# Performance work log

Measured on AMD Instinct MI355X. Metric: run time of the kernel, lower is better.

## Reference

```python
import jax, jax.numpy as jnp
import numpy as np

EPS = 1e-8  # torch.nn.CosineSimilarity default eps


def setup_inputs() -> dict:
    key = jax.random.key(0)
    k1, k2, k3 = jax.random.split(key, 3)
    B, T, D, L = 16, 256, 512, 32
    v1 = jax.random.normal(k1, (B, T, D), dtype=jnp.float32)
    v1_mask = jnp.ones((B, T), dtype=jnp.float32)
    v2 = jax.random.normal(k2, (B, D), dtype=jnp.float32)
    w = jax.random.normal(k3, (L, D), dtype=jnp.float32)
    return {"v1": v1, "v1_mask": v1_mask, "v2": v2, "w": w}


def reference(v1, v1_mask, v2, w):
    # v1: [B,T,D], v1_mask: [B,T], v2: [B,D], w: [L,D]
    # Original math: cos over D of (w * v1) and (w * v2), per perspective l.
    # Fused: (w_l*a)\cdot(w_l*b) = sum_d w[l,d]^2 a[d] b[d]; likewise for norms.
    v1m = v1 * v1_mask[:, :, None]              # [B,T,D]
    w2 = w * w                                   # [L,D]
    num = jnp.einsum('btd,ld,bd->btl', v1m, w2, v2)          # [B,T,L]
    n1 = jnp.sqrt(jnp.einsum('btd,ld->btl', v1m * v1m, w2))  # [B,T,L]
    n2 = jnp.sqrt(jnp.einsum('bd,ld->bl', v2 * v2, w2))      # [B,L]
    denom = jnp.maximum(n1 * n2[:, None, :], EPS)
    return num / denom                           # [B,T,L]
```

## Files before the change

### kernel.cpp

```cpp
#include <hip/hip_runtime.h>
#include <cstddef>

#define BB      16
#define TDIM    256
#define DDIM    512
#define LDIM    32
#define TROWS   16
#define NTHREADS 1024
#define EPSV    1e-8f

__global__ __launch_bounds__(NTHREADS, 1) void fullmatch_kernel(
    const float* __restrict__ v1,
    const float* __restrict__ v1_mask,
    const float* __restrict__ v2,
    const float* __restrict__ w,
    float* __restrict__ out)
{
    const int tid  = threadIdx.x;
    const int b    = blockIdx.x >> 4;
    const int tgrp = blockIdx.x & 15;
    const int t0b  = tgrp * TROWS;

    const int dq = tid & 31;
    const int l  = tid >> 5;

    __shared__ float v1s[TROWS][DDIM];
    __shared__ float otile[TROWS][LDIM];

    float4 w2r[4], hr[4];
    float n2p = 0.f;
    {
        const float* __restrict__ wrow = w  + (size_t)l * DDIM;
        const float* __restrict__ v2b  = v2 + (size_t)b * DDIM;
        #pragma unroll
        for (int j = 0; j < 4; ++j) {
            const int d = dq * 4 + j * 128;
            const float4 wv = *(const float4*)(wrow + d);
            const float4 vv = *(const float4*)(v2b + d);
            float4 w2;
            w2.x = wv.x * wv.x; w2.y = wv.y * wv.y;
            w2.z = wv.z * wv.z; w2.w = wv.w * wv.w;
            w2r[j] = w2;
            float4 h;
            h.x = w2.x * vv.x; h.y = w2.y * vv.y;
            h.z = w2.z * vv.z; h.w = w2.w * vv.w;
            hr[j] = h;
            n2p = fmaf(h.x, vv.x, n2p);
            n2p = fmaf(h.y, vv.y, n2p);
            n2p = fmaf(h.z, vv.z, n2p);
            n2p = fmaf(h.w, vv.w, n2p);
        }
    }

    #pragma unroll
    for (int k = 0; k < 2; ++k) {
        const int f = tid + k * NTHREADS;
        const int r = f >> 7;
        const int q = f & 127;
        const float4 val = *(const float4*)(v1 + (size_t)(b * TDIM + t0b + r) * DDIM + q * 4);
        const float  mk  = v1_mask[b * TDIM + t0b + r];
        float4 o;
        o.x = val.x * mk; o.y = val.y * mk; o.z = val.z * mk; o.w = val.w * mk;
        *(float4*)(&v1s[r][q * 4]) = o;
    }
    __syncthreads();

    float accN[TROWS], accD[TROWS];
    #pragma unroll
    for (int t = 0; t < TROWS; ++t) { accN[t] = 0.f; accD[t] = 0.f; }

    #pragma unroll
    for (int j = 0; j < 4; ++j) {
        const float4 w2 = w2r[j];
        const float4 h  = hr[j];
        const float* __restrict__ base = &v1s[0][dq * 4 + j * 128];
        #pragma unroll
        for (int t = 0; t < TROWS; ++t) {
            const float4 a = *(const float4*)(base + t * DDIM);
            accN[t] = fmaf(a.x, h.x, accN[t]);
            accN[t] = fmaf(a.y, h.y, accN[t]);
            accN[t] = fmaf(a.z, h.z, accN[t]);
            accN[t] = fmaf(a.w, h.w, accN[t]);
            accD[t] = fmaf(a.x * a.x, w2.x, accD[t]);
            accD[t] = fmaf(a.y * a.y, w2.y, accD[t]);
            accD[t] = fmaf(a.z * a.z, w2.z, accD[t]);
            accD[t] = fmaf(a.w * a.w, w2.w, accD[t]);
        }
    }

    #pragma unroll
    for (int m = 16; m >= 1; m >>= 1) {
        n2p += __shfl_xor(n2p, m, 64);
        #pragma unroll
        for (int t = 0; t < TROWS; ++t) {
            accN[t] += __shfl_xor(accN[t], m, 64);
            accD[t] += __shfl_xor(accD[t], m, 64);
        }
    }

    if (dq == 0) {
        const float n2v = sqrtf(n2p);
        #pragma unroll
        for (int t = 0; t < TROWS; ++t) {
            const float den = fmaxf(sqrtf(accD[t]) * n2v, EPSV);
            otile[t][l] = accN[t] / den;
        }
    }
    __syncthreads();

    if (tid < (TROWS * LDIM) / 4) {
        const size_t base = (size_t)(b * TDIM + t0b) * LDIM;
        *(float4*)(out + base + tid * 4) = *(const float4*)(&otile[0][0] + tid * 4);
    }
}

extern "C" void kernel_launch(void* const* d_in, const int* in_sizes, int n_in,
                              void* d_out, int out_size, void* d_ws, size_t ws_size,
                              hipStream_t stream) {
    const float* v1      = (const float*)d_in[0];
    const float* v1_mask = (const float*)d_in[1];
    const float* v2      = (const float*)d_in[2];
    const float* w       = (const float*)d_in[3];
    float* out           = (float*)d_out;

    const dim3 grid(BB * (TDIM / TROWS));
    const dim3 block(NTHREADS);
    fullmatch_kernel<<<grid, block, 0, stream>>>(v1, v1_mask, v2, w, out);
}
```

Baseline: 21.73 us.

## Rewrite as thread-per-row kernel with async LDS double-buffering and readlane weight broadcast

Replaces the 1024-thread block with a 256-thread block where each lane owns one time row and each wave handles two perspectives. v1 is streamed in four D-chunks into double-buffered LDS using global_load_lds with an XOR swizzle, and the w^2 and h terms are broadcast with readlane. Because each lane accumulates its own row, the per-row cross-lane shuffle reduction goes away. The mask is applied algebraically in the epilogue, and block IDs are remapped so each XCD gets a group of tiles. The cost is that every block reloads the full v1 tile once for each of its four perspective groups, adding redundant global traffic, and the readlane-heavy inner loop puts more pressure on scalar registers.

```diff
diff --git a/kernel.cpp b/kernel.cpp
--- a/kernel.cpp
+++ b/kernel.cpp
@@ -1,15 +1,17 @@
 #include <hip/hip_runtime.h>
 #include <cstddef>
 
-#define BB      16
-#define TDIM    256
-#define DDIM    512
-#define LDIM    32
-#define TROWS   16
-#define NTHREADS 1024
-#define EPSV    1e-8f
+#define EPSV 1e-8f
 
-__global__ __launch_bounds__(NTHREADS, 1) void fullmatch_kernel(
+__device__ __forceinline__ float rdlane(float x, int s) {
+    return __int_as_float(__builtin_amdgcn_readlane(__float_as_int(x), s));
+}
+
+#define GLD16(gp, lp) \
+    __builtin_amdgcn_global_load_lds((const __attribute__((address_space(1))) void*)(gp), \
+                                     (__attribute__((address_space(3))) void*)(lp), 16, 0, 0)
+
+__global__ __launch_bounds__(256, 1) void fullmatch_kernel(
     const float* __restrict__ v1,
     const float* __restrict__ v1_mask,
     const float* __restrict__ v2,
@@ -17,101 +19,129 @@
     float* __restrict__ out)
 {
     const int tid  = threadIdx.x;
-    const int b    = blockIdx.x >> 4;
-    const int tgrp = blockIdx.x & 15;
-    const int t0b  = tgrp * TROWS;
+    const int lane = tid & 63;
+    const int wv   = tid >> 6;
 
-    const int dq = tid & 31;
-    const int l  = tid >> 5;
+    const int bid   = blockIdx.x;
+    const int xcd   = bid & 7;
+    const int slot  = bid >> 3;
+    const int tileg = xcd * 8 + (slot >> 2);
+    const int lg    = slot & 3;
+    const int b  = tileg >> 2;
+    const int tc = tileg & 3;
+    const int t0 = tc * 64;
+    const int p  = lg * 4 + wv;
+    const int t  = t0 + lane;
 
-    __shared__ float v1s[TROWS][DDIM];
-    __shared__ float otile[TROWS][LDIM];
+    __shared__ float v1s[2][64][128];
 
-    float4 w2r[4], hr[4];
-    float n2p = 0.f;
+    const size_t v1base = (size_t)(b * 256 + t0) * 512;
+
+    #pragma unroll
+    for (int j = 0; j < 8; ++j) {
+        const int r0 = (wv * 8 + j) * 2;
+        const int r  = r0 + (lane >> 5);
+        const int c4 = (lane & 31) ^ (r & 31);
+        GLD16(v1 + v1base + (size_t)r * 512 + c4 * 4, &v1s[0][r0][0]);
+    }
+
+    float4 w2A[2], w2B[2], hA[2], hB[2];
+    float n2pA = 0.f, n2pB = 0.f;
     {
-        const float* __restrict__ wrow = w  + (size_t)l * DDIM;
-        const float* __restrict__ v2b  = v2 + (size_t)b * DDIM;
+        const float* __restrict__ v2b = v2 + (size_t)b * 512;
+        const float* __restrict__ wAp = w + (size_t)p * 512;
+        const float* __restrict__ wBp = w + (size_t)(p + 16) * 512;
         #pragma unroll
-        for (int j = 0; j < 4; ++j) {
-            const int d = dq * 4 + j * 128;
-            const float4 wv = *(const float4*)(wrow + d);
-            const float4 vv = *(const float4*)(v2b + d);
-            float4 w2;
-            w2.x = wv.x * wv.x; w2.y = wv.y * wv.y;
-            w2.z = wv.z * wv.z; w2.w = wv.w * wv.w;
-            w2r[j] = w2;
-            float4 h;
-            h.x = w2.x * vv.x; h.y = w2.y * vv.y;
-            h.z = w2.z * vv.z; h.w = w2.w * vv.w;
-            hr[j] = h;
-            n2p = fmaf(h.x, vv.x, n2p);
-            n2p = fmaf(h.y, vv.y, n2p);
-            n2p = fmaf(h.z, vv.z, n2p);
-            n2p = fmaf(h.w, vv.w, n2p);
+        for (int q = 0; q < 2; ++q) {
+            const int k4 = q * 64 + lane;
+            const float4 wa = *(const float4*)(wAp + k4 * 4);
+            const float4 wb = *(const float4*)(wBp + k4 * 4);
+            const float4 vv = *(const float4*)(v2b + k4 * 4);
+            float4 sa, sb, ha, hb;
+            sa.x = wa.x*wa.x; sa.y = wa.y*wa.y; sa.z = wa.z*wa.z; sa.w = wa.w*wa.w;
+            sb.x = wb.x*wb.x; sb.y = wb.y*wb.y; sb.z = wb.z*wb.z; sb.w = wb.w*wb.w;
+            ha.x = sa.x*vv.x; ha.y = sa.y*vv.y; ha.z = sa.z*vv.z; ha.w = sa.w*vv.w;
+            hb.x = sb.x*vv.x; hb.y = sb.y*vv.y; hb.z = sb.z*vv.z; hb.w = sb.w*vv.w;
+            w2A[q] = sa; w2B[q] = sb; hA[q] = ha; hB[q] = hb;
+            n2pA += ha.x*vv.x + ha.y*vv.y + ha.z*vv.z + ha.w*vv.w;
+            n2pB += hb.x*vv.x + hb.y*vv.y + hb.z*vv.z + hb.w*vv.w;
+        }
+    }
+    #pragma unroll
+    for (int m = 32; m >= 1; m >>= 1) {
+        n2pA += __shfl_xor(n2pA, m, 64);
+        n2pB += __shfl_xor(n2pB, m, 64);
+    }
+    const float n2vA = sqrtf(n2pA);
+    const float n2vB = sqrtf(n2pB);
+    const float mk   = v1_mask[b * 256 + t];
+
+    float accNA = 0.f, accNB = 0.f, accDA = 0.f, accDB = 0.f;
+
+    #pragma unroll
+    for (int c = 0; c < 4; ++c) {
+        __syncthreads();
+        if (c < 3) {
+            #pragma unroll
+            for (int j = 0; j < 8; ++j) {
+                const int r0 = (wv * 8 + j) * 2;
+                const int r  = r0 + (lane >> 5);
+                const int c4 = (lane & 31) ^ (r & 31);
+                GLD16(v1 + v1base + (size_t)r * 512 + (c + 1) * 128 + c4 * 4,
+                      &v1s[(c + 1) & 1][r0][0]);
+            }
+        }
+        const float* __restrict__ row = &v1s[c & 1][lane][0];
+        const int lm = lane & 31;
+        #pragma unroll 8
+        for (int s = 0; s < 32; ++s) {
+            const float4 a = *(const float4*)(row + ((s ^ lm) << 2));
+            const int li = ((c & 1) << 5) + s;
+            const float wax = rdlane(w2A[c >> 1].x, li);
+            const float way = rdlane(w2A[c >> 1].y, li);
+            const float waz = rdlane(w2A[c >> 1].z, li);
+            const float waw = rdlane(w2A[c >> 1].w, li);
+            const float wbx = rdlane(w2B[c >> 1].x, li);
+            const float wby = rdlane(w2B[c >> 1].y, li);
+            const float wbz = rdlane(w2B[c >> 1].z, li);
+            const float wbw = rdlane(w2B[c >> 1].w, li);
+            const float hax = rdlane(hA[c >> 1].x, li);
+            const float hay = rdlane(hA[c >> 1].y, li);
+            const float haz = rdlane(hA[c >> 1].z, li);
+            const float haw = rdlane(hA[c >> 1].w, li);
+            const float hbx = rdlane(hB[c >> 1].x, li);
+            const float hby = rdlane(hB[c >> 1].y, li);
+            const float hbz = rdlane(hB[c >> 1].z, li);
+            const float hbw = rdlane(hB[c >> 1].w, li);
+
+            const float x2 = a.x * a.x, y2 = a.y * a.y;
+            const float z2 = a.z * a.z, q2 = a.w * a.w;
+
+            accNA = fmaf(a.x, hax, accNA);
+            accNA = fmaf(a.y, hay, accNA);
+            accNA = fmaf(a.z, haz, accNA);
+            accNA = fmaf(a.w, haw, accNA);
+            accNB = fmaf(a.x, hbx, accNB);
+            accNB = fmaf(a.y, hby, accNB);
+            accNB = fmaf(a.z, hbz, accNB);
+            accNB = fmaf(a.w, hbw, accNB);
+            accDA = fmaf(x2, wax, accDA);
+            accDA = fmaf(y2, way, accDA);
+            accDA = fmaf(z2, waz, accDA);
+            accDA = fmaf(q2, waw, accDA);
+            accDB = fmaf(x2, wbx, accDB);
+            accDB = fmaf(y2, wby, accDB);
+            accDB = fmaf(z2, wbz, accDB);
+            accDB = fmaf(q2, wbw, accDB);
         }
     }
 
-    #pragma unroll
-    for (int k = 0; k < 2; ++k) {
-        const int f = tid + k * NTHREADS;
-        const int r = f >> 7;
-        const int q = f & 127;
-        const float4 val = *(const float4*)(v1 + (size_t)(b * TDIM + t0b + r) * DDIM + q * 4);
-        const float  mk  = v1_mask[b * TDIM + t0b + r];
-        float4 o;
-        o.x = val.x * mk; o.y = val.y * mk; o.z = val.z * mk; o.w = val.w * mk;
-        *(float4*)(&v1s[r][q * 4]) = o;
-    }
-    __syncthreads();
-
-    float accN[TROWS], accD[TROWS];
-    #pragma unroll
-    for (int t = 0; t < TROWS; ++t) { accN[t] = 0.f; accD[t] = 0.f; }
-
-    #pragma unroll
-    for (int j = 0; j < 4; ++j) {
-        const float4 w2 = w2r[j];
-        const float4 h  = hr[j];
-        const float* __restrict__ base = &v1s[0][dq * 4 + j * 128];
-        #pragma unroll
-        for (int t = 0; t < TROWS; ++t) {
-            const float4 a = *(const float4*)(base + t * DDIM);
-            accN[t] = fmaf(a.x, h.x, accN[t]);
-            accN[t] = fmaf(a.y, h.y, accN[t]);
-            accN[t] = fmaf(a.z, h.z, accN[t]);
-            accN[t] = fmaf(a.w, h.w, accN[t]);
-            accD[t] = fmaf(a.x * a.x, w2.x, accD[t]);
-            accD[t] = fmaf(a.y * a.y, w2.y, accD[t]);
-            accD[t] = fmaf(a.z * a.z, w2.z, accD[t]);
-            accD[t] = fmaf(a.w * a.w, w2.w, accD[t]);
-        }
-    }
-
-    #pragma unroll
-    for (int m = 16; m >= 1; m >>= 1) {
-        n2p += __shfl_xor(n2p, m, 64);
-        #pragma unroll
-        for (int t = 0; t < TROWS; ++t) {
-            accN[t] += __shfl_xor(accN[t], m, 64);
-            accD[t] += __shfl_xor(accD[t], m, 64);
-        }
-    }
-
-    if (dq == 0) {
-        const float n2v = sqrtf(n2p);
-        #pragma unroll
-        for (int t = 0; t < TROWS; ++t) {
-            const float den = fmaxf(sqrtf(accD[t]) * n2v, EPSV);
-            otile[t][l] = accN[t] / den;
-        }
-    }
-    __syncthreads();
-
-    if (tid < (TROWS * LDIM) / 4) {
-        const size_t base = (size_t)(b * TDIM + t0b) * LDIM;
-        *(float4*)(out + base + tid * 4) = *(const float4*)(&otile[0][0] + tid * 4);
-    }
+    const float amk  = fabsf(mk);
+    const float denA = fmaxf(sqrtf(accDA) * amk * n2vA, EPSV);
+    const float denB = fmaxf(sqrtf(accDB) * amk * n2vB, EPSV);
+    const size_t o = (size_t)(b * 256 + t) * 32;
+    out[o + p]      = (accNA * mk) / denA;
+    out[o + p + 16] = (accNB * mk) / denB;
 }
 
 extern "C" void kernel_launch(void* const* d_in, const int* in_sizes, int n_in,
@@ -123,7 +153,5 @@
     const float* w       = (const float*)d_in[3];
     float* out           = (float*)d_out;
 
-    const dim3 grid(BB * (TDIM / TROWS));
-    const dim3 block(NTHREADS);
-    fullmatch_kernel<<<grid, block, 0, stream>>>(v1, v1_mask, v2, w, out);
+    fullmatch_kernel<<<dim3(256), dim3(256), 0, stream>>>(v1, v1_mask, v2, w, out);
 }
```

Result: faster. 21.25 us (-2.2%).
